# Kernel tuning notes

Measured on AMD Instinct MI355X. Metric: run time of the kernel, lower is better.

Reference implementation:

```python
import jax, jax.numpy as jnp
import numpy as np

D = 512      # d_model
H = 8        # n_heads
HD = D // H  # head_dim = 64
PS = 4       # patch_size
B, T, P = 4, 4096, 1024


def setup_inputs() -> dict:
    key = jax.random.key(0)
    ks = jax.random.split(key, 12)
    s = 1.0 / np.sqrt(D)
    return {
        "token_hidden": jax.random.normal(ks[0], (B, T, D), jnp.float32),
        "patch_hidden": jax.random.normal(ks[1], (B, P, D), jnp.float32),
        "Wq": jax.random.normal(ks[2], (D, D), jnp.float32) * s,
        "Wk": jax.random.normal(ks[3], (D, D), jnp.float32) * s,
        "Wv": jax.random.normal(ks[4], (D, D), jnp.float32) * s,
        "bq": jax.random.normal(ks[5], (D,), jnp.float32) * 0.02,
        "bk": jax.random.normal(ks[6], (D,), jnp.float32) * 0.02,
        "bv": jax.random.normal(ks[7], (D,), jnp.float32) * 0.02,
        "Wo": jax.random.normal(ks[8], (D, D), jnp.float32) * s,
        "bo": jax.random.normal(ks[9], (D,), jnp.float32) * 0.02,
    }


def reference(token_hidden, patch_hidden, Wq, Wk, Wv, bq, bk, bv, Wo, bo):
    b, t, _ = token_hidden.shape
    p = patch_hidden.shape[1]
    # QKV projections (equivalent to nn.MultiheadAttention in_proj)
    q = (token_hidden @ Wq + bq).reshape(b, t, H, HD)
    k = (patch_hidden @ Wk + bk).reshape(b, p, H, HD)
    v = (patch_hidden @ Wv + bv).reshape(b, p, H, HD)
    # scaled dot-product scores: [b, h, t, p]
    scores = jnp.einsum('bthd,bphd->bhtp', q, k) / jnp.sqrt(jnp.asarray(HD, q.dtype))
    # block-causal token-to-patch mask: token i attends to patches 0..i//PS
    allowed = jnp.arange(p)[None, :] <= (jnp.arange(t)[:, None] // PS)  # [t, p]
    scores = jnp.where(allowed[None, None, :, :], scores, -jnp.inf)
    attn = jax.nn.softmax(scores, axis=-1)
    ctx = jnp.einsum('bhtp,bphd->bthd', attn, v).reshape(b, t, D)
    out = ctx @ Wo + bo  # out_proj
    return token_hidden + out
```

## Files before the change

kernel.cpp:

```cpp
#include <hip/hip_runtime.h>
#include <stdint.h>

#define DM 512
#define NH 8
#define HDIM 64
#define TT 4096
#define PP 1024

typedef float f32x4 __attribute__((ext_vector_type(4)));
typedef __bf16 bf16x8 __attribute__((ext_vector_type(8)));
typedef unsigned short u16x8 __attribute__((ext_vector_type(8)));
typedef unsigned short u16x4 __attribute__((ext_vector_type(4)));

static __device__ __forceinline__ unsigned short f2bf(float f) {
  unsigned u = __builtin_bit_cast(unsigned, f);
  u += 0x7fff + ((u >> 16) & 1);
  return (unsigned short)(u >> 16);
}

static __device__ __forceinline__ void load_lds16(const void* g, void* l) {
  __builtin_amdgcn_global_load_lds(
      (__attribute__((address_space(1))) void*)g,
      (__attribute__((address_space(3))) void*)l, 16, 0, 0);
}

static __device__ __forceinline__ f32x4 mfma16(bf16x8 a, bf16x8 b, f32x4 c) {
  return __builtin_amdgcn_mfma_f32_16x16x32_bf16(a, b, c, 0, 0, 0);
}

__global__ __launch_bounds__(256) void k_convert(
    const float* __restrict__ tok, const float* __restrict__ pat,
    const float* __restrict__ wq, const float* __restrict__ wk,
    const float* __restrict__ wv, const float* __restrict__ wo,
    unsigned short* __restrict__ xtok, unsigned short* __restrict__ xpat,
    unsigned short* __restrict__ wt) {
  const int gid = blockIdx.x * 256 + threadIdx.x;
  const int NX = 2621440;
  if (gid < NX) {
    int i4 = gid * 4;
    const float* src;
    unsigned short* dst;
    int idx;
    if (i4 < 8388608) { src = tok; dst = xtok; idx = i4; }
    else              { src = pat; dst = xpat; idx = i4 - 8388608; }
    f32x4 v = *(const f32x4*)&src[idx];
    u16x4 o;
#pragma unroll
    for (int i = 0; i < 4; ++i) o[i] = f2bf(v[i]);
    *(u16x4*)&dst[idx] = o;
  } else {
    int wi = gid - NX;
    int wid = wi >> 16;
    int e = (wi & 65535) << 2;
    int k = e >> 9, n = e & 511;
    const float* w = (wid == 0) ? wq : (wid == 1) ? wk : (wid == 2) ? wv : wo;
    f32x4 v = *(const f32x4*)&w[e];
    unsigned short* wtb = wt + (wid << 18);
#pragma unroll
    for (int i = 0; i < 4; ++i) wtb[(n + i) * 512 + k] = f2bf(v[i]);
  }
}

__device__ __forceinline__ void gemm_body(
    const unsigned short* __restrict__ A, const unsigned short* __restrict__ Wt,
    const float* __restrict__ bias, unsigned short* __restrict__ outb,
    float* __restrict__ outf, const float* __restrict__ resid, int mode,
    int bid, unsigned short* sA, unsigned short* sB) {
  const int tid = threadIdx.x;
  const int wave = tid >> 6, lane = tid & 63;
  const int q = lane >> 4, c = lane & 15;
  const int bm = bid >> 2, bn = bid & 3;
  const int wm = (wave >> 1) * 64, wn = (wave & 1) * 64;
  const int lr = lane >> 2, lc = (lane & 3) * 8;

  f32x4 acc[4][4];
#pragma unroll
  for (int i = 0; i < 4; ++i)
#pragma unroll
    for (int j = 0; j < 4; ++j) acc[i][j] = (f32x4){0.f, 0.f, 0.f, 0.f};

  const int rowA0 = bm * 128, rowB0 = bn * 128;

  for (int k0 = 0; k0 < 512; k0 += 32) {
#pragma unroll
    for (int qq = 0; qq < 2; ++qq) {
      const int chunk = wave * 2 + qq;
      load_lds16(&A[(rowA0 + chunk * 16 + lr) * 512 + k0 + lc], &sA[chunk * 512]);
      load_lds16(&Wt[(rowB0 + chunk * 16 + lr) * 512 + k0 + lc], &sB[chunk * 512]);
    }
    __syncthreads();
    bf16x8 af[4], bfr[4];
#pragma unroll
    for (int mt = 0; mt < 4; ++mt)
      af[mt] = __builtin_bit_cast(bf16x8, *(const u16x8*)&sA[(wm + mt * 16 + c) * 32 + q * 8]);
#pragma unroll
    for (int nt = 0; nt < 4; ++nt)
      bfr[nt] = __builtin_bit_cast(bf16x8, *(const u16x8*)&sB[(wn + nt * 16 + c) * 32 + q * 8]);
#pragma unroll
    for (int mt = 0; mt < 4; ++mt)
#pragma unroll
      for (int nt = 0; nt < 4; ++nt)
        acc[mt][nt] = mfma16(af[mt], bfr[nt], acc[mt][nt]);
    __syncthreads();
  }

#pragma unroll
  for (int nt = 0; nt < 4; ++nt) {
    const int col = bn * 128 + wn + nt * 16 + c;
    const float bcol = bias[col];
#pragma unroll
    for (int mt = 0; mt < 4; ++mt) {
      const int row0 = bm * 128 + wm + mt * 16 + q * 4;
#pragma unroll
      for (int r = 0; r < 4; ++r) {
        const int row = row0 + r;
        const float v = acc[mt][nt][r] + bcol;
        if (mode == 3) {
          const int o = row * 512 + col;
          outf[o] = v + resid[o];
        } else if (mode == 2) {
          outb[((row >> 10) << 19) + (col << 10) + (row & 1023)] = f2bf(v);
        } else {
          outb[row * 512 + col] = f2bf(v);
        }
      }
    }
  }
}

__global__ __launch_bounds__(256) void k_gemm(
    const unsigned short* __restrict__ A, const unsigned short* __restrict__ Wt,
    const float* __restrict__ bias, unsigned short* __restrict__ outb,
    float* __restrict__ outf, const float* __restrict__ resid, int mode) {
  __shared__ unsigned short sA[128 * 32];
  __shared__ unsigned short sB[128 * 32];
  gemm_body(A, Wt, bias, outb, outf, resid, mode, blockIdx.x, sA, sB);
}

__global__ __launch_bounds__(256) void k_gemm_kv(
    const unsigned short* __restrict__ A,
    const unsigned short* __restrict__ WtK, const unsigned short* __restrict__ WtV,
    const float* __restrict__ bk, const float* __restrict__ bv,
    unsigned short* __restrict__ KB, unsigned short* __restrict__ VTB) {
  __shared__ unsigned short sA[128 * 32];
  __shared__ unsigned short sB[128 * 32];
  const int kv = blockIdx.x >> 7;
  const int bid = blockIdx.x & 127;
  if (kv == 0)
    gemm_body(A, WtK, bk, KB, nullptr, nullptr, 1, bid, sA, sB);
  else
    gemm_body(A, WtV, bv, VTB, nullptr, nullptr, 2, bid, sA, sB);
}

__global__ __launch_bounds__(256) void k_attn(
    const unsigned short* __restrict__ Q,
    const unsigned short* __restrict__ K,
    const unsigned short* __restrict__ VT,
    unsigned short* __restrict__ CTX) {
  __shared__ unsigned short sK[32 * 80];
  __shared__ unsigned short sV[64 * 40];

  const int tid = threadIdx.x;
  const int lane = tid & 63;
  const int wave = tid >> 6;
  const int q = lane >> 4, c = lane & 15;

  const int tg = 63 - (blockIdx.x >> 5);
  const int bh = blockIdx.x & 31;
  const int b = bh >> 3, h = bh & 7;
  const int t0 = tg * 64 + wave * 16;
  const int t = t0 + c;

  const int qbase = (b * TT + t) * 512 + h * 64 + q * 8;
  const bf16x8 qf0 = __builtin_bit_cast(bf16x8, *(const u16x8*)&Q[qbase]);
  const bf16x8 qf1 = __builtin_bit_cast(bf16x8, *(const u16x8*)&Q[qbase + 32]);

  f32x4 octx[4];
#pragma unroll
  for (int i = 0; i < 4; ++i) octx[i] = (f32x4){0.f, 0.f, 0.f, 0.f};
  float m_run = -1e30f, l_run = 0.f;

  const int limit = t >> 2;
  const int ntile = ((tg * 16 + 15) >> 5) + 1;

  const int krow = tid >> 3, kcol = (tid & 7) * 8;
  const int vrow = tid >> 2, vcol = (tid & 3) * 8;
  const int kgbase = (b * PP + krow) * 512 + h * 64 + kcol;
  const int vgbase = (b << 19) + ((h * 64 + vrow) << 10) + vcol;

  for (int pt = 0; pt < ntile; ++pt) {
    const int p0 = pt * 32;
    const u16x8 kreg = *(const u16x8*)&K[kgbase + p0 * 512];
    const u16x8 vreg = *(const u16x8*)&VT[vgbase + p0];
    __syncthreads();
    *(u16x8*)&sK[krow * 80 + kcol] = kreg;
    *(u16x8*)&sV[vrow * 40 + vcol] = vreg;
    __syncthreads();

    f32x4 s0 = (f32x4){0.f, 0.f, 0.f, 0.f};
    f32x4 s1 = s0;
    {
      const bf16x8 ka0 = __builtin_bit_cast(bf16x8, *(const u16x8*)&sK[c * 80 + q * 8]);
      const bf16x8 ka1 = __builtin_bit_cast(bf16x8, *(const u16x8*)&sK[c * 80 + 32 + q * 8]);
      const bf16x8 kb0 = __builtin_bit_cast(bf16x8, *(const u16x8*)&sK[(16 + c) * 80 + q * 8]);
      const bf16x8 kb1 = __builtin_bit_cast(bf16x8, *(const u16x8*)&sK[(16 + c) * 80 + 32 + q * 8]);
      s0 = mfma16(ka0, qf0, s0);
      s0 = mfma16(ka1, qf1, s0);
      s1 = mfma16(kb0, qf0, s1);
      s1 = mfma16(kb1, qf1, s1);
    }
    s0 *= 0.125f;
    s1 *= 0.125f;
    if (p0 + 31 > (t0 >> 2)) {
#pragma unroll
      for (int r = 0; r < 4; ++r) {
        if (p0 + q * 4 + r > limit) s0[r] = -1e30f;
        if (p0 + 16 + q * 4 + r > limit) s1[r] = -1e30f;
      }
    }
    float tmax = fmaxf(fmaxf(fmaxf(s0[0], s0[1]), fmaxf(s0[2], s0[3])),
                       fmaxf(fmaxf(s1[0], s1[1]), fmaxf(s1[2], s1[3])));
    tmax = fmaxf(tmax, __shfl_xor(tmax, 16));
    tmax = fmaxf(tmax, __shfl_xor(tmax, 32));
    const float m_new = fmaxf(m_run, tmax);
    const float alpha = __expf(m_run - m_new);
    m_run = m_new;
    float pv0[4], pv1[4], tsum = 0.f;
#pragma unroll
    for (int r = 0; r < 4; ++r) {
      pv0[r] = __expf(s0[r] - m_new);
      pv1[r] = __expf(s1[r] - m_new);
      tsum += pv0[r] + pv1[r];
    }
    tsum += __shfl_xor(tsum, 16);
    tsum += __shfl_xor(tsum, 32);
    l_run = l_run * alpha + tsum;
#pragma unroll
    for (int mt = 0; mt < 4; ++mt) octx[mt] *= alpha;

    u16x8 bp;
#pragma unroll
    for (int j = 0; j < 8; ++j) {
      const int src = (((q & 1) * 2 + (j >> 2)) << 4) | c;
      const float v0 = __shfl(pv0[j & 3], src);
      const float v1 = __shfl(pv1[j & 3], src);
      bp[j] = f2bf((q >= 2) ? v1 : v0);
    }
    const bf16x8 pb = __builtin_bit_cast(bf16x8, bp);

#pragma unroll
    for (int mt = 0; mt < 4; ++mt) {
      const bf16x8 vf =
          __builtin_bit_cast(bf16x8, *(const u16x8*)&sV[(mt * 16 + c) * 40 + q * 8]);
      octx[mt] = mfma16(vf, pb, octx[mt]);
    }
  }

  const float inv = 1.f / l_run;
  const int obase = (b * TT + t) * 512 + h * 64 + q * 4;
#pragma unroll
  for (int mt = 0; mt < 4; ++mt) {
    u16x4 o;
#pragma unroll
    for (int r = 0; r < 4; ++r) o[r] = f2bf(octx[mt][r] * inv);
    *(u16x4*)&CTX[obase + mt * 16] = o;
  }
}

extern "C" void kernel_launch(void* const* d_in, const int* in_sizes, int n_in,
                              void* d_out, int out_size, void* d_ws, size_t ws_size,
                              hipStream_t stream) {
  const float* tok = (const float*)d_in[0];
  const float* pat = (const float*)d_in[1];
  const float* Wq = (const float*)d_in[2];
  const float* Wk = (const float*)d_in[3];
  const float* Wv = (const float*)d_in[4];
  const float* bq = (const float*)d_in[5];
  const float* bk = (const float*)d_in[6];
  const float* bv = (const float*)d_in[7];
  const float* Wo = (const float*)d_in[8];
  const float* bo = (const float*)d_in[9];
  float* out = (float*)d_out;

  unsigned short* ws = (unsigned short*)d_ws;
  unsigned short* XTOK = ws;
  unsigned short* XPAT = ws + 8388608;
  unsigned short* WT = ws + 10485760;
  unsigned short* QB = ws + 11534336;
  unsigned short* KB = ws + 19922944;
  unsigned short* VTB = ws + 22020096;

  k_convert<<<11264, 256, 0, stream>>>(tok, pat, Wq, Wk, Wv, Wo, XTOK, XPAT, WT);
  k_gemm<<<512, 256, 0, stream>>>(XTOK, WT, bq, QB, nullptr, nullptr, 0);
  k_gemm_kv<<<256, 256, 0, stream>>>(XPAT, WT + 262144, WT + 524288, bk, bv, KB, VTB);
  k_attn<<<2048, 256, 0, stream>>>(QB, KB, VTB, XTOK);
  k_gemm<<<512, 256, 0, stream>>>(XTOK, WT + 786432, bo, nullptr, out, tok, 3);
}
```

Measured before the change: 234.4 us.

## Drop online softmax max, double query rows per wave, compute row sums via MFMA

The attention kernel drops the running-max online softmax: scores are exponentiated directly, the 1/sqrt(d) scale is folded into the Q projection epilogue, and row sums come from an MFMA against a vector of ones. Each wave now handles 32 query rows instead of 16, which halves the grid and reuses each loaded K/V tile twice. Probabilities are repacked for the PV MFMA through a per-wave LDS buffer instead of cross-lane shuffles, and tile order alternates short and long rows to balance the causal workload. Skipping max subtraction removes reductions and rescaling, but exp can overflow if scores are large, and the new bf16 packing rounds half-up instead of to nearest even.

```diff
diff --git a/kernel.cpp b/kernel.cpp
--- a/kernel.cpp
+++ b/kernel.cpp
@@ -11,11 +11,18 @@
 typedef __bf16 bf16x8 __attribute__((ext_vector_type(8)));
 typedef unsigned short u16x8 __attribute__((ext_vector_type(8)));
 typedef unsigned short u16x4 __attribute__((ext_vector_type(4)));
+typedef unsigned int u32x2 __attribute__((ext_vector_type(2)));
 
 static __device__ __forceinline__ unsigned short f2bf(float f) {
   unsigned u = __builtin_bit_cast(unsigned, f);
   u += 0x7fff + ((u >> 16) & 1);
   return (unsigned short)(u >> 16);
+}
+
+static __device__ __forceinline__ unsigned packbf(float a, float b) {
+  unsigned ua = __builtin_bit_cast(unsigned, a) + 0x8000u;
+  unsigned ub = __builtin_bit_cast(unsigned, b) + 0x8000u;
+  return __builtin_amdgcn_perm(ub, ua, 0x07060302u);
 }
 
 static __device__ __forceinline__ void load_lds16(const void* g, void* l) {
@@ -104,6 +111,7 @@
     __syncthreads();
   }
 
+  const float vs = (mode == 0) ? 0.125f : 1.0f;
 #pragma unroll
   for (int nt = 0; nt < 4; ++nt) {
     const int col = bn * 128 + wn + nt * 16 + c;
@@ -114,7 +122,7 @@
 #pragma unroll
       for (int r = 0; r < 4; ++r) {
         const int row = row0 + r;
-        const float v = acc[mt][nt][r] + bcol;
+        const float v = (acc[mt][nt][r] + bcol) * vs;
         if (mode == 3) {
           const int o = row * 512 + col;
           outf[o] = v + resid[o];
@@ -159,111 +167,125 @@
     unsigned short* __restrict__ CTX) {
   __shared__ unsigned short sK[32 * 80];
   __shared__ unsigned short sV[64 * 40];
+  __shared__ unsigned short sPT[4 * 32 * 40];
 
   const int tid = threadIdx.x;
   const int lane = tid & 63;
   const int wave = tid >> 6;
   const int q = lane >> 4, c = lane & 15;
 
-  const int tg = 63 - (blockIdx.x >> 5);
+  const int i = blockIdx.x >> 5;
+  const int tg = (i & 1) ? (31 - (i >> 1)) : (i >> 1);
   const int bh = blockIdx.x & 31;
   const int b = bh >> 3, h = bh & 7;
-  const int t0 = tg * 64 + wave * 16;
-  const int t = t0 + c;
-
-  const int qbase = (b * TT + t) * 512 + h * 64 + q * 8;
-  const bf16x8 qf0 = __builtin_bit_cast(bf16x8, *(const u16x8*)&Q[qbase]);
-  const bf16x8 qf1 = __builtin_bit_cast(bf16x8, *(const u16x8*)&Q[qbase + 32]);
-
-  f32x4 octx[4];
-#pragma unroll
-  for (int i = 0; i < 4; ++i) octx[i] = (f32x4){0.f, 0.f, 0.f, 0.f};
-  float m_run = -1e30f, l_run = 0.f;
-
-  const int limit = t >> 2;
-  const int ntile = ((tg * 16 + 15) >> 5) + 1;
-
+  const int t0 = tg * 128 + wave * 32;
+  const int tA = t0 + c, tB = t0 + 16 + c;
+
+  const int qbA = (b * TT + tA) * 512 + h * 64 + q * 8;
+  const int qbB = (b * TT + tB) * 512 + h * 64 + q * 8;
+  const bf16x8 qfA0 = __builtin_bit_cast(bf16x8, *(const u16x8*)&Q[qbA]);
+  const bf16x8 qfA1 = __builtin_bit_cast(bf16x8, *(const u16x8*)&Q[qbA + 32]);
+  const bf16x8 qfB0 = __builtin_bit_cast(bf16x8, *(const u16x8*)&Q[qbB]);
+  const bf16x8 qfB1 = __builtin_bit_cast(bf16x8, *(const u16x8*)&Q[qbB + 32]);
+
+  f32x4 oA[4], oB[4];
+#pragma unroll
+  for (int m = 0; m < 4; ++m) {
+    oA[m] = (f32x4){0.f, 0.f, 0.f, 0.f};
+    oB[m] = (f32x4){0.f, 0.f, 0.f, 0.f};
+  }
+  f32x4 lA = (f32x4){0.f, 0.f, 0.f, 0.f};
+  f32x4 lB = lA;
+  const u16x8 onesu = {0x3F80, 0x3F80, 0x3F80, 0x3F80, 0x3F80, 0x3F80, 0x3F80, 0x3F80};
+  const bf16x8 ones = __builtin_bit_cast(bf16x8, onesu);
+
+  const int ntile = tg + 1;
   const int krow = tid >> 3, kcol = (tid & 7) * 8;
   const int vrow = tid >> 2, vcol = (tid & 3) * 8;
-  const int kgbase = (b * PP + krow) * 512 + h * 64 + kcol;
-  const int vgbase = (b << 19) + ((h * 64 + vrow) << 10) + vcol;
+  const int kg = (b * PP + krow) * 512 + h * 64 + kcol;
+  const int vg = (b << 19) + ((h * 64 + vrow) << 10) + vcol;
+  unsigned short* sp = &sPT[wave * 1280];
 
   for (int pt = 0; pt < ntile; ++pt) {
     const int p0 = pt * 32;
-    const u16x8 kreg = *(const u16x8*)&K[kgbase + p0 * 512];
-    const u16x8 vreg = *(const u16x8*)&VT[vgbase + p0];
+    const u16x8 kreg = *(const u16x8*)&K[kg + p0 * 512];
+    const u16x8 vreg = *(const u16x8*)&VT[vg + p0];
     __syncthreads();
     *(u16x8*)&sK[krow * 80 + kcol] = kreg;
     *(u16x8*)&sV[vrow * 40 + vcol] = vreg;
     __syncthreads();
 
-    f32x4 s0 = (f32x4){0.f, 0.f, 0.f, 0.f};
-    f32x4 s1 = s0;
+    const bf16x8 ka0 = __builtin_bit_cast(bf16x8, *(const u16x8*)&sK[c * 80 + q * 8]);
+    const bf16x8 ka1 = __builtin_bit_cast(bf16x8, *(const u16x8*)&sK[c * 80 + 32 + q * 8]);
+    const bf16x8 kb0 = __builtin_bit_cast(bf16x8, *(const u16x8*)&sK[(16 + c) * 80 + q * 8]);
+    const bf16x8 kb1 = __builtin_bit_cast(bf16x8, *(const u16x8*)&sK[(16 + c) * 80 + 32 + q * 8]);
+
+    const f32x4 z = (f32x4){0.f, 0.f, 0.f, 0.f};
+    f32x4 sA0 = mfma16(ka1, qfA1, mfma16(ka0, qfA0, z));
+    f32x4 sA1 = mfma16(kb1, qfA1, mfma16(kb0, qfA0, z));
+    f32x4 sB0 = mfma16(ka1, qfB1, mfma16(ka0, qfB0, z));
+    f32x4 sB1 = mfma16(kb1, qfB1, mfma16(kb0, qfB0, z));
+
+    if (pt + 1 == ntile) {
+      const int limA = tA >> 2, limB = tB >> 2;
+      const int pb0 = p0 + q * 4, pb1 = p0 + 16 + q * 4;
+#pragma unroll
+      for (int r = 0; r < 4; ++r) {
+        if (pb0 + r > limA) sA0[r] = -1e30f;
+        if (pb1 + r > limA) sA1[r] = -1e30f;
+        if (pb0 + r > limB) sB0[r] = -1e30f;
+        if (pb1 + r > limB) sB1[r] = -1e30f;
+      }
+    }
+
+    float pA0[4], pA1[4], pB0[4], pB1[4];
+#pragma unroll
+    for (int r = 0; r < 4; ++r) {
+      pA0[r] = __expf(sA0[r]);
+      pA1[r] = __expf(sA1[r]);
+      pB0[r] = __expf(sB0[r]);
+      pB1[r] = __expf(sB1[r]);
+    }
+
     {
-      const bf16x8 ka0 = __builtin_bit_cast(bf16x8, *(const u16x8*)&sK[c * 80 + q * 8]);
-      const bf16x8 ka1 = __builtin_bit_cast(bf16x8, *(const u16x8*)&sK[c * 80 + 32 + q * 8]);
-      const bf16x8 kb0 = __builtin_bit_cast(bf16x8, *(const u16x8*)&sK[(16 + c) * 80 + q * 8]);
-      const bf16x8 kb1 = __builtin_bit_cast(bf16x8, *(const u16x8*)&sK[(16 + c) * 80 + 32 + q * 8]);
-      s0 = mfma16(ka0, qf0, s0);
-      s0 = mfma16(ka1, qf1, s0);
-      s1 = mfma16(kb0, qf0, s1);
-      s1 = mfma16(kb1, qf1, s1);
-    }
-    s0 *= 0.125f;
-    s1 *= 0.125f;
-    if (p0 + 31 > (t0 >> 2)) {
-#pragma unroll
-      for (int r = 0; r < 4; ++r) {
-        if (p0 + q * 4 + r > limit) s0[r] = -1e30f;
-        if (p0 + 16 + q * 4 + r > limit) s1[r] = -1e30f;
-      }
-    }
-    float tmax = fmaxf(fmaxf(fmaxf(s0[0], s0[1]), fmaxf(s0[2], s0[3])),
-                       fmaxf(fmaxf(s1[0], s1[1]), fmaxf(s1[2], s1[3])));
-    tmax = fmaxf(tmax, __shfl_xor(tmax, 16));
-    tmax = fmaxf(tmax, __shfl_xor(tmax, 32));
-    const float m_new = fmaxf(m_run, tmax);
-    const float alpha = __expf(m_run - m_new);
-    m_run = m_new;
-    float pv0[4], pv1[4], tsum = 0.f;
-#pragma unroll
-    for (int r = 0; r < 4; ++r) {
-      pv0[r] = __expf(s0[r] - m_new);
-      pv1[r] = __expf(s1[r] - m_new);
-      tsum += pv0[r] + pv1[r];
-    }
-    tsum += __shfl_xor(tsum, 16);
-    tsum += __shfl_xor(tsum, 32);
-    l_run = l_run * alpha + tsum;
-#pragma unroll
-    for (int mt = 0; mt < 4; ++mt) octx[mt] *= alpha;
-
-    u16x8 bp;
-#pragma unroll
-    for (int j = 0; j < 8; ++j) {
-      const int src = (((q & 1) * 2 + (j >> 2)) << 4) | c;
-      const float v0 = __shfl(pv0[j & 3], src);
-      const float v1 = __shfl(pv1[j & 3], src);
-      bp[j] = f2bf((q >= 2) ? v1 : v0);
-    }
-    const bf16x8 pb = __builtin_bit_cast(bf16x8, bp);
+      u32x2 w;
+      w[0] = packbf(pA0[0], pA0[1]); w[1] = packbf(pA0[2], pA0[3]);
+      *(u32x2*)&sp[c * 40 + q * 4] = w;
+      w[0] = packbf(pA1[0], pA1[1]); w[1] = packbf(pA1[2], pA1[3]);
+      *(u32x2*)&sp[c * 40 + 16 + q * 4] = w;
+      w[0] = packbf(pB0[0], pB0[1]); w[1] = packbf(pB0[2], pB0[3]);
+      *(u32x2*)&sp[(16 + c) * 40 + q * 4] = w;
+      w[0] = packbf(pB1[0], pB1[1]); w[1] = packbf(pB1[2], pB1[3]);
+      *(u32x2*)&sp[(16 + c) * 40 + 16 + q * 4] = w;
+    }
+    const bf16x8 pbA = __builtin_bit_cast(bf16x8, *(const u16x8*)&sp[c * 40 + q * 8]);
+    const bf16x8 pbB = __builtin_bit_cast(bf16x8, *(const u16x8*)&sp[(16 + c) * 40 + q * 8]);
 
 #pragma unroll
     for (int mt = 0; mt < 4; ++mt) {
       const bf16x8 vf =
           __builtin_bit_cast(bf16x8, *(const u16x8*)&sV[(mt * 16 + c) * 40 + q * 8]);
-      octx[mt] = mfma16(vf, pb, octx[mt]);
-    }
-  }
-
-  const float inv = 1.f / l_run;
-  const int obase = (b * TT + t) * 512 + h * 64 + q * 4;
+      oA[mt] = mfma16(vf, pbA, oA[mt]);
+      oB[mt] = mfma16(vf, pbB, oB[mt]);
+    }
+    lA = mfma16(ones, pbA, lA);
+    lB = mfma16(ones, pbB, lB);
+  }
+
+  const float invA = 1.f / lA[0];
+  const float invB = 1.f / lB[0];
+  const int obA = (b * TT + tA) * 512 + h * 64 + q * 4;
+  const int obB = (b * TT + tB) * 512 + h * 64 + q * 4;
 #pragma unroll
   for (int mt = 0; mt < 4; ++mt) {
-    u16x4 o;
-#pragma unroll
-    for (int r = 0; r < 4; ++r) o[r] = f2bf(octx[mt][r] * inv);
-    *(u16x4*)&CTX[obase + mt * 16] = o;
+    u16x4 oa, ob;
+#pragma unroll
+    for (int r = 0; r < 4; ++r) {
+      oa[r] = f2bf(oA[mt][r] * invA);
+      ob[r] = f2bf(oB[mt][r] * invB);
+    }
+    *(u16x4*)&CTX[obA + mt * 16] = oa;
+    *(u16x4*)&CTX[obB + mt * 16] = ob;
   }
 }
 
@@ -293,6 +315,6 @@
   k_convert<<<11264, 256, 0, stream>>>(tok, pat, Wq, Wk, Wv, Wo, XTOK, XPAT, WT);
   k_gemm<<<512, 256, 0, stream>>>(XTOK, WT, bq, QB, nullptr, nullptr, 0);
   k_gemm_kv<<<256, 256, 0, stream>>>(XPAT, WT + 262144, WT + 524288, bk, bv, KB, VTB);
-  k_attn<<<2048, 256, 0, stream>>>(QB, KB, VTB, XTOK);
+  k_attn<<<1024, 256, 0, stream>>>(QB, KB, VTB, XTOK);
   k_gemm<<<512, 256, 0, stream>>>(XTOK, WT + 786432, bo, nullptr, out, tok, 3);
 }
```

Result: faster. 227.3 us (-3.0%).
